# Performance work log

Measured on AMD Instinct MI355X. Metric: run time of the kernel, lower is better.

## Reference

```python
import jax, jax.numpy as jnp
import numpy as np

B, T, C = 2, 1024, 2048
HEAD = 64              # args.head_size_a
H = C // HEAD          # n_head = 32
D_DECAY, D_AAA, D_MV, D_GATE = 96, 96, 64, 256
GN_EPS = 0.00064
EPS_NORM = 1e-12

ARGS = ['x', 'v0', 'xx_r', 'xx_w', 'xx_k', 'xx_v', 'xx_a', 'xx_g',
        'ww_b', 'ww_w1', 'ww_w2', 'aa_b', 'aa_w1', 'aa_w2',
        'vv_b', 'vv_w1', 'vv_w2', 'gg_w1', 'gg_w2',
        'kk_s', 'ka_s', 'rk_s', 'W_r', 'W_k', 'W_v', 'W_o', 'gn_w', 'gn_b']


def setup_inputs() -> dict:
    key = jax.random.key(0)
    it = iter(jax.random.split(key, 32))
    nrm = lambda shape, s=1.0: jax.random.normal(next(it), shape, jnp.float32) * s
    d = {'x': nrm((B, T, C)), 'v0': nrm((B, T, C))}
    for nm in ('xx_r', 'xx_w', 'xx_k', 'xx_v', 'xx_a', 'xx_g',
               'ww_b', 'aa_b', 'vv_b', 'kk_s', 'ka_s'):
        d[nm] = nrm((1, 1, C), 0.5)
    d['ww_w1'] = nrm((C, D_DECAY), 0.02); d['ww_w2'] = nrm((D_DECAY, C), 0.02)
    d['aa_w1'] = nrm((C, D_AAA), 0.02);   d['aa_w2'] = nrm((D_AAA, C), 0.02)
    d['vv_w1'] = nrm((C, D_MV), 0.02);    d['vv_w2'] = nrm((D_MV, C), 0.02)
    d['gg_w1'] = nrm((C, D_GATE), 0.02);  d['gg_w2'] = nrm((D_GATE, C), 0.02)
    d['rk_s'] = nrm((H, HEAD), 0.5)
    d['W_r'] = nrm((C, C), 0.02); d['W_k'] = nrm((C, C), 0.02)
    d['W_v'] = nrm((C, C), 0.02); d['W_o'] = nrm((C, C), 0.02)
    d['gn_w'] = jnp.ones((C,), jnp.float32)
    d['gn_b'] = jnp.zeros((C,), jnp.float32)
    return d


def _rwkv7_op(r, w, k, v, a, b):
    # RWKV7 state recurrence: state[b,h,i,j] (i = value dim, j = key dim),
    # vectorized over (B,H,N), scanned over T.
    to_tbhn = lambda t: t.reshape(B, T, H, HEAD).astype(jnp.float32).transpose(1, 0, 2, 3)
    rT, kT, vT, aT, bT = map(to_tbhn, (r, k, v, a, b))
    wT = jnp.exp(-jnp.exp(to_tbhn(w)))   # decay in (0, 1)
    state0 = jnp.zeros((B, H, HEAD, HEAD), jnp.float32)

    def step(state, inp):
        wt, kt, vt, at, bt, rt = inp     # each [B,H,N]
        sa = jnp.einsum('bhij,bhj->bhi', state, at)
        state = (state * wt[:, :, None, :]
                 + sa[..., None] * bt[:, :, None, :]
                 + vt[..., None] * kt[:, :, None, :])
        return state, jnp.einsum('bhij,bhj->bhi', state, rt)

    _, outs = jax.lax.scan(step, state0, (wT, kT, vT, aT, bT, rT))  # [T,B,H,N]
    return outs.transpose(1, 0, 2, 3).reshape(B, T, C)


def _group_norm(y, gn_w, gn_b):
    # GroupNorm(H, C, eps=0.00064) applied on (B*T, C): per-(token, head) stats over N
    yh = y.reshape(B, T, H, HEAD)
    mu = yh.mean(-1, keepdims=True)
    var = yh.var(-1, keepdims=True)
    yh = (yh - mu) * jax.lax.rsqrt(var + GN_EPS)
    yh = yh * gn_w.reshape(1, 1, H, HEAD) + gn_b.reshape(1, 1, H, HEAD)
    return yh.reshape(B, T, C)


def _forward(x, v0, xx_r, xx_w, xx_k, xx_v, xx_a, xx_g,
             ww_b, ww_w1, ww_w2, aa_b, aa_w1, aa_w2,
             vv_b, vv_w1, vv_w2, gg_w1, gg_w2,
             kk_s, ka_s, rk_s, W_r, W_k, W_v, W_o, gn_w, gn_b):
    # time_shift(x) - x : shift sequence right by one with zero pad
    xx = jnp.pad(x, ((0, 0), (1, 0), (0, 0)))[:, :T, :] - x
    xr = x + xx * xx_r; xw = x + xx * xx_w; xk = x + xx * xx_k
    xv = x + xx * xx_v; xa = x + xx * xx_a; xg = x + xx * xx_g

    r = xr @ W_r
    w = -jax.nn.softplus(-(ww_b + jnp.tanh(xw @ ww_w1) @ ww_w2)) - 0.5  # clamp to (-inf,-0.5)
    k = xk @ W_k
    v = xv @ W_v
    # layer_id > 0: mix with layer-0 value residual
    v = v + (v0 - v) * jax.nn.sigmoid(vv_b + (xv @ vv_w1) @ vv_w2)
    a = jax.nn.sigmoid(aa_b + (xa @ aa_w1) @ aa_w2)
    g = jax.nn.sigmoid(xg @ gg_w1) @ gg_w2

    kk = k * kk_s
    kkh = kk.reshape(B, T, H, HEAD)
    kk = (kkh / jnp.maximum(jnp.linalg.norm(kkh, axis=-1, keepdims=True), EPS_NORM)).reshape(B, T, C)
    k = k * (1.0 + (a - 1.0) * ka_s)

    y = _rwkv7_op(r, w, k, v, -kk, kk * a)
    y = _group_norm(y, gn_w, gn_b)
    # per-head bonus: (r*k*rk_s).sum(-1) * v
    bonus = ((r.reshape(B, T, H, HEAD) * k.reshape(B, T, H, HEAD) * rk_s).sum(-1, keepdims=True)
             * v.reshape(B, T, H, HEAD)).reshape(B, T, C)
    y = y + bonus
    return (y * g) @ W_o


def reference(x, v0, xx_r, xx_w, xx_k, xx_v, xx_a, xx_g,
              ww_b, ww_w1, ww_w2, aa_b, aa_w1, aa_w2,
              vv_b, vv_w1, vv_w2, gg_w1, gg_w2,
              kk_s, ka_s, rk_s, W_r, W_k, W_v, W_o, gn_w, gn_b):
    out = _forward(x, v0, xx_r, xx_w, xx_k, xx_v, xx_a, xx_g,
                   ww_b, ww_w1, ww_w2, aa_b, aa_w1, aa_w2,
                   vv_b, vv_w1, vv_w2, gg_w1, gg_w2,
                   kk_s, ka_s, rk_s, W_r, W_k, W_v, W_o, gn_w, gn_b)
    # layer_id > 0 passes v0 through unchanged
    return (out, v0)
```

## Files before the change

### kernel.cpp

```cpp
#include <hip/hip_runtime.h>
#include <hip/hip_bf16.h>
#include <math.h>

typedef unsigned short u16;
typedef __attribute__((ext_vector_type(4))) unsigned short us4;
typedef __attribute__((ext_vector_type(8))) unsigned short us8;
typedef __attribute__((ext_vector_type(8))) short s8v;
typedef __attribute__((ext_vector_type(4))) float f4v;

#define BB 2
#define TT 1024
#define CC 2048
#define HH 32
#define BT (BB*TT)


__device__ __forceinline__ float bf2f(u16 u) {
  return __uint_as_float(((unsigned int)u) << 16);
}
__device__ __forceinline__ u16 f2bf(float f) {
  unsigned int x = __float_as_uint(f);
  x += 0x7fffu + ((x >> 16) & 1u);
  return (u16)(x >> 16);
}

__device__ __forceinline__ void gload16(const u16* g, u16* l) {
  __builtin_amdgcn_global_load_lds(
      (const __attribute__((address_space(1))) void*)g,
      (__attribute__((address_space(3))) void*)l, 16, 0, 0);
}

__global__ __launch_bounds__(256)
void mix_k(const float* __restrict__ x, const float* __restrict__ s,
           u16* __restrict__ out) {
  int idx = blockIdx.x * 256 + threadIdx.x;
  int c = idx & (CC - 1);
  int t = (idx >> 11) & (TT - 1);
  float xv = x[idx];
  float xp = (t == 0) ? 0.f : x[idx - CC];
  out[idx] = f2bf(xv + (xp - xv) * s[c]);
}

__global__ __launch_bounds__(256)
void wt_k(const float* __restrict__ W, u16* __restrict__ Wt, int K, int N,
          int Kp) {
  __shared__ u16 tile[32][36];
  const int k0 = blockIdx.x * 32, n0 = blockIdx.y * 32;
  const int tid = threadIdx.x;
  const int r = tid >> 3, c4 = (tid & 7) << 2;
  float4 v = *(const float4*)(W + (size_t)(k0 + r) * N + n0 + c4);
  tile[r][c4 + 0] = f2bf(v.x); tile[r][c4 + 1] = f2bf(v.y);
  tile[r][c4 + 2] = f2bf(v.z); tile[r][c4 + 3] = f2bf(v.w);
  __syncthreads();
  ushort4 o;
  o.x = tile[c4 + 0][r]; o.y = tile[c4 + 1][r];
  o.z = tile[c4 + 2][r]; o.w = tile[c4 + 3][r];
  *(ushort4*)(Wt + (size_t)(n0 + r) * Kp + k0 + c4) = o;
}

enum { EPI_BF = 0, EPI_F32 = 1, EPI_BIAS_SP = 2, EPI_BIAS_SIG = 3,
       EPI_VMIX = 4 };

template<int EPI>
__global__ __launch_bounds__(256)
void mgemm_k(const u16* __restrict__ A, const u16* __restrict__ Bt,
             float* __restrict__ outF, u16* __restrict__ outB,
             int M, int N, int K, int lda, int ldb,
             const float* __restrict__ bias, const u16* __restrict__ p1,
             const float* __restrict__ p2)
{
  __shared__ alignas(16) u16 As[128 * 64];
  __shared__ alignas(16) u16 Bs[128 * 64];
  const int m0 = blockIdx.x * 128;
  const int n0 = blockIdx.y * 128;
  const int tid = threadIdx.x;
  const int lane = tid & 63;
  const int wid = tid >> 6;
  const int wr = wid >> 1, wc = wid & 1;
  f4v acc[4][4];
  #pragma unroll
  for (int i = 0; i < 4; ++i)
    #pragma unroll
    for (int j = 0; j < 4; ++j) acc[i][j] = f4v{0.f, 0.f, 0.f, 0.f};

  const int l15 = lane & 15;
  const int lq = lane >> 4;
  const int nkt = K >> 6;
  for (int kt = 0; kt < nkt; ++kt) {
    const int k0 = kt << 6;
    __syncthreads();
    #pragma unroll
    for (int a = 0; a < 4; ++a) {
      const int blkU = (wid * 4 + a) * 64;
      const int U = blkU + lane;
      const int row = U >> 3;
      const int u = U & 7;
      const int col = ((u ^ (row & 7)) << 3);
      gload16(A  + (size_t)(m0 + row) * lda + k0 + col, &As[blkU * 8]);
      gload16(Bt + (size_t)(n0 + row) * ldb + k0 + col, &Bs[blkU * 8]);
    }
    __syncthreads();
    #pragma unroll
    for (int h = 0; h < 2; ++h) {
      s8v af[4], bfr[4];
      #pragma unroll
      for (int i = 0; i < 4; ++i) {
        const int row = wr * 64 + i * 16 + l15;
        const int u = (h * 4 + lq) ^ (row & 7);
        af[i] = *(const s8v*)&As[row * 64 + u * 8];
      }
      #pragma unroll
      for (int j = 0; j < 4; ++j) {
        const int row = wc * 64 + j * 16 + l15;
        const int u = (h * 4 + lq) ^ (row & 7);
        bfr[j] = *(const s8v*)&Bs[row * 64 + u * 8];
      }
      #pragma unroll
      for (int i = 0; i < 4; ++i)
        #pragma unroll
        for (int j = 0; j < 4; ++j)
          acc[i][j] = __builtin_amdgcn_mfma_f32_16x16x32_bf16(af[i], bfr[j],
                                                              acc[i][j],
                                                              0, 0, 0);
    }
  }
  const int rbase = m0 + wr * 64 + (lq << 2);
  const int cbase = n0 + wc * 64 + l15;
  #pragma unroll
  for (int i = 0; i < 4; ++i) {
    #pragma unroll
    for (int j = 0; j < 4; ++j) {
      f4v c = acc[i][j];
      const int col = cbase + j * 16;
      #pragma unroll
      for (int q = 0; q < 4; ++q) {
        const int row = rbase + i * 16 + q;
        const size_t idx = (size_t)row * N + col;
        const float r = c[q];
        if (EPI == EPI_BF) {
          outB[idx] = f2bf(r);
        } else if (EPI == EPI_F32) {
          outF[idx] = r;
        } else if (EPI == EPI_BIAS_SP) {
          float u = bias[col] + r;
          float z = -u;
          float sp = fmaxf(z, 0.f) + log1pf(expf(-fabsf(z)));
          outB[idx] = f2bf(-sp - 0.5f);
        } else if (EPI == EPI_BIAS_SIG) {
          float u = bias[col] + r;
          outB[idx] = f2bf(1.f / (1.f + expf(-u)));
        } else if (EPI == EPI_VMIX) {
          float u = bias[col] + r;
          float sg = 1.f / (1.f + expf(-u));
          float v = bf2f(p1[idx]);
          float v0v = p2[idx];
          outB[idx] = f2bf(v + (v0v - v) * sg);
        }
      }
    }
  }
}

__global__ __launch_bounds__(256)
void gemm_part_k(const u16* __restrict__ A, const float* __restrict__ W,
                 float* __restrict__ outF, int M, int N, int K, int kchunk,
                 int NP)
{
  __shared__ alignas(16) float As[16][68];
  __shared__ alignas(16) float Bs[16][68];
  const int m0 = blockIdx.x * 64;
  const int n0 = blockIdx.y * 64;
  const int kz = blockIdx.z;
  const int k0base = kz * kchunk;
  const int tid = threadIdx.x;
  const int tx = tid & 15, ty = tid >> 4;
  float acc[4][4] = {{0.f}};
  const int a_m = tid >> 2;
  const int a_k = (tid & 3) << 2;
  const int b_k = tid >> 4;
  const int b_n = (tid & 15) << 2;
  const int niters = kchunk >> 4;
  for (int it = 0; it < niters; ++it) {
    const int k0 = k0base + (it << 4);
    float4 av;
    {
      ushort4 u = *(const ushort4*)(A + (size_t)(m0 + a_m) * K + (k0 + a_k));
      av = make_float4(bf2f(u.x), bf2f(u.y), bf2f(u.z), bf2f(u.w));
    }
    float4 bv;
    {
      int gn = n0 + b_n;
      const float* wp = W + (size_t)(k0 + b_k) * N + gn;
      if (gn + 3 < N) {
        bv = *(const float4*)wp;
      } else {
        bv.x = (gn + 0 < N) ? wp[0] : 0.f;
        bv.y = (gn + 1 < N) ? wp[1] : 0.f;
        bv.z = (gn + 2 < N) ? wp[2] : 0.f;
        bv.w = (gn + 3 < N) ? wp[3] : 0.f;
      }
    }
    __syncthreads();
    As[a_k + 0][a_m] = av.x; As[a_k + 1][a_m] = av.y;
    As[a_k + 2][a_m] = av.z; As[a_k + 3][a_m] = av.w;
    Bs[b_k][b_n + 0] = bv.x; Bs[b_k][b_n + 1] = bv.y;
    Bs[b_k][b_n + 2] = bv.z; Bs[b_k][b_n + 3] = bv.w;
    __syncthreads();
    #pragma unroll
    for (int kk = 0; kk < 16; ++kk) {
      float4 a4 = *(const float4*)&As[kk][ty << 2];
      float4 b4 = *(const float4*)&Bs[kk][tx << 2];
      float ar[4] = {a4.x, a4.y, a4.z, a4.w};
      float br[4] = {b4.x, b4.y, b4.z, b4.w};
      #pragma unroll
      for (int i = 0; i < 4; ++i)
        #pragma unroll
        for (int j = 0; j < 4; ++j)
          acc[i][j] = fmaf(ar[i], br[j], acc[i][j]);
    }
  }
  #pragma unroll
  for (int i = 0; i < 4; ++i) {
    int gm = m0 + (ty << 2) + i;
    #pragma unroll
    for (int j = 0; j < 4; ++j) {
      int gn = n0 + (tx << 2) + j;
      if (gn >= N) continue;
      outF[((size_t)kz * M + gm) * NP + gn] = acc[i][j];
    }
  }
}

__global__ __launch_bounds__(256)
void reduce_k(const float* __restrict__ part, u16* __restrict__ out,
              int M, int D, int NP, int nz, int act, int Dp)
{
  int idx = blockIdx.x * 256 + threadIdx.x;
  if (idx >= M * Dp) return;
  int t = idx / Dp, n = idx - t * Dp;
  float s = 0.f;
  if (n < D) {
    for (int z = 0; z < nz; ++z) s += part[((size_t)z * M + t) * NP + n];
    if (act == 1) s = tanhf(s);
    else if (act == 2) s = 1.f / (1.f + expf(-s));
  }
  out[idx] = f2bf(s);
}

__global__ __launch_bounds__(256)
void prep_k(const u16* __restrict__ k_in, const u16* __restrict__ a_in,
            const u16* __restrict__ r_in, const u16* __restrict__ w_in,
            const float* __restrict__ kk_s, const float* __restrict__ ka_s,
            u16* __restrict__ ao_out, u16* __restrict__ bo_out,
            u16* __restrict__ k_out, u16* __restrict__ wd_out,
            u16* __restrict__ rw_out, float2* __restrict__ scal)
{
  int tid = threadIdx.x;
  int lane = tid & 63;
  int wv = tid >> 6;
  int hidx = blockIdx.x * 4 + wv;
  int h = hidx & (HH - 1);
  int c = (h << 6) + lane;
  size_t base = ((size_t)hidx << 6) + lane;
  float k = bf2f(k_in[base]);
  float kk = k * kk_s[c];
  float ss = kk * kk;
  for (int off = 32; off; off >>= 1) ss += __shfl_xor(ss, off, 64);
  float kkn = kk / fmaxf(sqrtf(ss), 1e-12f);
  float a = bf2f(a_in[base]);
  float r = bf2f(r_in[base]);
  float kf = k * (1.f + (a - 1.f) * ka_s[c]);
  float wd = expf(-expf(bf2f(w_in[base])));
  float bo = kkn * a;
  ao_out[base] = f2bf(-kkn);
  bo_out[base] = f2bf(bo);
  k_out[base]  = f2bf(kf);
  wd_out[base] = f2bf(wd);
  rw_out[base] = f2bf(wd * r);
  float kr = kf * r, br = bo * r;
  kr += __shfl_xor(kr, 1, 64);  br += __shfl_xor(br, 1, 64);
  kr += __shfl_xor(kr, 2, 64);  br += __shfl_xor(br, 2, 64);
  kr += __shfl_xor(kr, 4, 64);  br += __shfl_xor(br, 4, 64);
  kr += __shfl_xor(kr, 8, 64);  br += __shfl_xor(br, 8, 64);
  kr += __shfl_xor(kr, 16, 64); br += __shfl_xor(br, 16, 64);
  kr += __shfl_xor(kr, 32, 64); br += __shfl_xor(br, 32, 64);
  if (lane == 0) scal[hidx] = make_float2(kr, br);
}

__global__ __launch_bounds__(256)
void prep2_k(u16* __restrict__ wd, u16* __restrict__ ao,
             u16* __restrict__ bo, u16* __restrict__ rw,
             const u16* __restrict__ kf, float4* __restrict__ scal4)
{
  int tid = threadIdx.x;
  int lane = tid & 63;
  int wv = tid >> 6;
  int hpidx = blockIdx.x * 4 + wv;
  int h = hpidx & (HH - 1);
  int btp = hpidx >> 5;
  int tp = btp & (TT / 2 - 1);
  int b = btp >> 9;
  size_t be = ((size_t)(b * TT + 2 * tp)) * CC + (h << 6) + lane;
  size_t bodd = be + CC;
  float wd1 = bf2f(wd[be]),  wd2 = bf2f(wd[bodd]);
  float ao2 = bf2f(ao[bodd]), rw2 = bf2f(rw[bodd]);
  float bo1 = bf2f(bo[be]),  k1  = bf2f(kf[be]);
  float cba = bo1 * ao2, ckb = k1 * ao2, crb = bo1 * rw2, crk = k1 * rw2;
  #pragma unroll
  for (int off = 32; off; off >>= 1) {
    cba += __shfl_xor(cba, off, 64);
    ckb += __shfl_xor(ckb, off, 64);
    crb += __shfl_xor(crb, off, 64);
    crk += __shfl_xor(crk, off, 64);
  }
  wd[be]   = f2bf(wd1 * wd2);
  wd[bodd] = f2bf(k1 * wd2);
  ao[bodd] = f2bf(wd1 * ao2);
  bo[be]   = f2bf(bo1 * wd2);
  rw[bodd] = f2bf(wd1 * rw2);
  if (lane == 0) scal4[hpidx] = make_float4(cba, ckb, crb, crk);
}

__global__ __launch_bounds__(256)
void rec_k(const u16* __restrict__ rw, const u16* __restrict__ wd,
           const u16* __restrict__ kv, const u16* __restrict__ v,
           const u16* __restrict__ ao, const u16* __restrict__ bo,
           const float2* __restrict__ scal, const float4* __restrict__ scal4,
           u16* __restrict__ y)
{
  const int gw = blockIdx.x * 4 + (threadIdx.x >> 6);
  const int lane = threadIdx.x & 63;
  const int sub = lane & 15;
  const int grp = lane >> 4;
  const int bh = gw >> 4;
  const int rblk = gw & 15;
  const int i = rblk * 4 + grp;
  const int b = bh >> 5, h = bh & (HH - 1);
  const size_t base0 = ((size_t)b * TT) * CC + (h << 6);
  const size_t vecb = base0 + (sub << 2);
  const size_t vb   = base0 + i;
  const int sbase = b * TT * HH + h;
  const int pbase = b * (TT / 2) * HH + h;
  float s0 = 0.f, s1 = 0.f, s2 = 0.f, s3 = 0.f;

  us4 W12, KW1, AO1, WA2, BW1, BO2, RW1, WR2, K2;
  float V1, V2; float2 SE, SO; float4 S4;
#define PLOAD(TP) do {                                                  \
    const size_t be_ = vecb + (size_t)(2 * (TP)) * CC;                  \
    const size_t bo_ = be_ + CC;                                        \
    W12 = *(const us4*)(wd + be_);  KW1 = *(const us4*)(wd + bo_);      \
    AO1 = *(const us4*)(ao + be_);  WA2 = *(const us4*)(ao + bo_);      \
    BW1 = *(const us4*)(bo + be_);  BO2 = *(const us4*)(bo + bo_);      \
    RW1 = *(const us4*)(rw + be_);  WR2 = *(const us4*)(rw + bo_);      \
    K2  = *(const us4*)(kv + bo_);                                      \
    V1 = bf2f(v[vb + (size_t)(2 * (TP)) * CC]);                         \
    V2 = bf2f(v[vb + (size_t)(2 * (TP) + 1) * CC]);                     \
    SE = scal[sbase + (2 * (TP)) * HH];                                 \
    SO = scal[sbase + (2 * (TP) + 1) * HH];                             \
    S4 = scal4[pbase + (TP) * HH];                                      \
  } while (0)

  PLOAD(0);
  for (int tp = 0; tp < TT / 2; ++tp) {
    const float w0 = bf2f(W12[0]), w1 = bf2f(W12[1]),
                w2 = bf2f(W12[2]), w3 = bf2f(W12[3]);
    const float kw0 = bf2f(KW1[0]), kw1_ = bf2f(KW1[1]),
                kw2 = bf2f(KW1[2]), kw3 = bf2f(KW1[3]);
    const float a0 = bf2f(AO1[0]), a1 = bf2f(AO1[1]),
                a2 = bf2f(AO1[2]), a3 = bf2f(AO1[3]);
    const float x0 = bf2f(WA2[0]), x1 = bf2f(WA2[1]),
                x2 = bf2f(WA2[2]), x3 = bf2f(WA2[3]);
    const float bw0 = bf2f(BW1[0]), bw1_ = bf2f(BW1[1]),
                bw2 = bf2f(BW1[2]), bw3 = bf2f(BW1[3]);
    const float b0 = bf2f(BO2[0]), b1 = bf2f(BO2[1]),
                b2 = bf2f(BO2[2]), b3 = bf2f(BO2[3]);
    const float e0 = bf2f(RW1[0]), e1 = bf2f(RW1[1]),
                e2 = bf2f(RW1[2]), e3 = bf2f(RW1[3]);
    const float f0 = bf2f(WR2[0]), f1 = bf2f(WR2[1]),
                f2 = bf2f(WR2[2]), f3 = bf2f(WR2[3]);
    const float k0 = bf2f(K2[0]), k1 = bf2f(K2[1]),
                k2 = bf2f(K2[2]), k3 = bf2f(K2[3]);
    const float v1c = V1, v2c = V2;
    const float kr1 = SE.x, br1 = SE.y, kr2 = SO.x, br2 = SO.y;
    const float cba = S4.x, ckb = S4.y, crb = S4.z, crk = S4.w;
    if (tp + 1 < TT / 2) PLOAD(tp + 1);
    float u1 = fmaf(s3, a3, fmaf(s2, a2, fmaf(s1, a1, s0 * a0)));
    float u2 = fmaf(s3, x3, fmaf(s2, x2, fmaf(s1, x1, s0 * x0)));
    float q1 = fmaf(s3, e3, fmaf(s2, e2, fmaf(s1, e1, s0 * e0)));
    float q2 = fmaf(s3, f3, fmaf(s2, f2, fmaf(s1, f1, s0 * f0)));
    u1 += __shfl_xor(u1, 1, 64);  u2 += __shfl_xor(u2, 1, 64);
    q1 += __shfl_xor(q1, 1, 64);  q2 += __shfl_xor(q2, 1, 64);
    u1 += __shfl_xor(u1, 2, 64);  u2 += __shfl_xor(u2, 2, 64);
    q1 += __shfl_xor(q1, 2, 64);  q2 += __shfl_xor(q2, 2, 64);
    u1 += __shfl_xor(u1, 4, 64);  u2 += __shfl_xor(u2, 4, 64);
    q1 += __shfl_xor(q1, 4, 64);  q2 += __shfl_xor(q2, 4, 64);
    u1 += __shfl_xor(u1, 8, 64);  u2 += __shfl_xor(u2, 8, 64);
    q1 += __shfl_xor(q1, 8, 64);  q2 += __shfl_xor(q2, 8, 64);
    const float sac = fmaf(ckb, v1c, fmaf(cba, u1, u2));
    const float y1 = fmaf(br1, u1, fmaf(kr1, v1c, q1));
    const float y2 = fmaf(br2, sac, fmaf(kr2, v2c,
                       fmaf(crb, u1, fmaf(crk, v1c, q2))));
    s0 = fmaf(v2c, k0, fmaf(v1c, kw0, fmaf(sac, b0, fmaf(u1, bw0, s0 * w0))));
    s1 = fmaf(v2c, k1, fmaf(v1c, kw1_, fmaf(sac, b1, fmaf(u1, bw1_, s1 * w1))));
    s2 = fmaf(v2c, k2, fmaf(v1c, kw2, fmaf(sac, b2, fmaf(u1, bw2, s2 * w2))));
    s3 = fmaf(v2c, k3, fmaf(v1c, kw3, fmaf(sac, b3, fmaf(u1, bw3, s3 * w3))));
    if (sub == 0) {
      y[vb + (size_t)(2 * tp) * CC] = f2bf(y1);
      y[vb + (size_t)(2 * tp + 1) * CC] = f2bf(y2);
    }
  }
#undef PLOAD
}

__global__ __launch_bounds__(256)
void gn_k(u16* __restrict__ y, const u16* __restrict__ r,
          const u16* __restrict__ k, const u16* __restrict__ v,
          const u16* __restrict__ g, const float* __restrict__ rk_s,
          const float* __restrict__ gn_w, const float* __restrict__ gn_b)
{
  int tid = threadIdx.x, lane = tid & 63, wv = tid >> 6;
  int hidx = blockIdx.x * 4 + wv;
  int h = hidx & (HH - 1);
  int c = (h << 6) + lane;
  size_t base = ((size_t)hidx << 6) + lane;
  float yv = bf2f(y[base]), rv = bf2f(r[base]), kv = bf2f(k[base]);
  float vv = bf2f(v[base]), gv = bf2f(g[base]);
  float bsum = rv * kv * rk_s[c];
  float s1 = yv, s2 = yv * yv;
  for (int off = 32; off; off >>= 1) {
    s1 += __shfl_xor(s1, off, 64);
    s2 += __shfl_xor(s2, off, 64);
    bsum += __shfl_xor(bsum, off, 64);
  }
  float mu = s1 * (1.f / 64.f);
  float var = s2 * (1.f / 64.f) - mu * mu;
  float rstd = rsqrtf(var + 0.00064f);
  float z = (yv - mu) * rstd * gn_w[c] + gn_b[c];
  y[base] = f2bf((z + bsum * vv) * gv);
}

__global__ __launch_bounds__(256)
void copy_v0(const float* __restrict__ v0, float* __restrict__ out) {
  int idx = blockIdx.x * 256 + threadIdx.x;
  ((float4*)out)[idx] = ((const float4*)v0)[idx];
}

__global__ __launch_bounds__(256)
void zero_out(float* __restrict__ out) {
  int idx = blockIdx.x * 256 + threadIdx.x;
  ((float4*)out)[idx] = make_float4(0.f, 0.f, 0.f, 0.f);
}

extern "C" void kernel_launch(void* const* d_in, const int* in_sizes, int n_in,
                              void* d_out, int out_size, void* d_ws, size_t ws_size,
                              hipStream_t stream) {
  (void)n_in; (void)out_size;
  const bool dictOrder = (in_sizes[9] == CC);
  int IX[28];
  if (dictOrder) {
    const int m[28] = {0,1,2,3,4,5,6,7, 8,13,14, 9,15,16, 10,17,18, 19,20,
                       11,12,21, 22,23,24,25, 26,27};
    for (int i = 0; i < 28; ++i) IX[i] = m[i];
  } else {
    for (int i = 0; i < 28; ++i) IX[i] = i;
  }
  const float* x     = (const float*)d_in[IX[0]];
  const float* v0    = (const float*)d_in[IX[1]];
  const float* xx_r  = (const float*)d_in[IX[2]];
  const float* xx_w  = (const float*)d_in[IX[3]];
  const float* xx_k  = (const float*)d_in[IX[4]];
  const float* xx_v  = (const float*)d_in[IX[5]];
  const float* xx_a  = (const float*)d_in[IX[6]];
  const float* xx_g  = (const float*)d_in[IX[7]];
  const float* ww_b  = (const float*)d_in[IX[8]];
  const float* ww_w1 = (const float*)d_in[IX[9]];
  const float* ww_w2 = (const float*)d_in[IX[10]];
  const float* aa_b  = (const float*)d_in[IX[11]];
  const float* aa_w1 = (const float*)d_in[IX[12]];
  const float* aa_w2 = (const float*)d_in[IX[13]];
  const float* vv_b  = (const float*)d_in[IX[14]];
  const float* vv_w1 = (const float*)d_in[IX[15]];
  const float* vv_w2 = (const float*)d_in[IX[16]];
  const float* gg_w1 = (const float*)d_in[IX[17]];
  const float* gg_w2 = (const float*)d_in[IX[18]];
  const float* kk_s  = (const float*)d_in[IX[19]];
  const float* ka_s  = (const float*)d_in[IX[20]];
  const float* rk_s  = (const float*)d_in[IX[21]];
  const float* W_r   = (const float*)d_in[IX[22]];
  const float* W_k   = (const float*)d_in[IX[23]];
  const float* W_v   = (const float*)d_in[IX[24]];
  const float* W_o   = (const float*)d_in[IX[25]];
  const float* gn_w  = (const float*)d_in[IX[26]];
  const float* gn_b  = (const float*)d_in[IX[27]];

  const size_t NBTC = (size_t)BT * CC;
  dim3 blk(256);
  const int grid4f = (int)(NBTC / 4 / 256);

  const size_t WS_NEED = 7 * NBTC * sizeof(u16);
  float* outF = (float*)d_out;
  if (ws_size < WS_NEED || d_ws == nullptr) {
    zero_out<<<grid4f, blk, 0, stream>>>(outF);
    copy_v0<<<grid4f, blk, 0, stream>>>(v0, outF + NBTC);
    return;
  }

  u16* W16   = (u16*)d_ws;
  u16* R0 = W16 + 0 * NBTC;
  u16* R1 = W16 + 1 * NBTC;
  u16* R2 = W16 + 2 * NBTC;
  u16* R3 = W16 + 3 * NBTC;
  u16* R4 = W16 + 4 * NBTC;
  u16* R5 = W16 + 5 * NBTC;
  u16* R6 = W16 + 6 * NBTC;
  float* partY = (float*)R3;
  float* partG = (float*)R5;
  u16* ws_y = (u16*)(outF + NBTC);
  float2* scal = (float2*)(ws_y + NBTC);
  float4* scal4 = (float4*)(ws_y + NBTC + (size_t)BT * HH * 4);

  const int gridMix = (BT * CC) / 256;
  dim3 gM(BT / 128, 2048 / 128);

  mix_k<<<gridMix, blk, 0, stream>>>(x, xx_w, R6);
  gemm_part_k<<<dim3(32, 2, 8), blk, 0, stream>>>(R6, ww_w1, partY,
      BT, 96, 2048, 256, 128);
  reduce_k<<<(BT * 128) / 256, blk, 0, stream>>>(partY, R0, BT, 96, 128, 8, 1, 128);
  wt_k<<<dim3(3, 64), blk, 0, stream>>>(ww_w2, R1, 96, 2048, 128);
  mgemm_k<EPI_BIAS_SP><<<gM, blk, 0, stream>>>(R0, R1, nullptr, R5,
      BT, 2048, 128, 128, 128, ww_b, nullptr, nullptr);

  mix_k<<<gridMix, blk, 0, stream>>>(x, xx_a, R6);
  gemm_part_k<<<dim3(32, 2, 8), blk, 0, stream>>>(R6, aa_w1, partY,
      BT, 96, 2048, 256, 128);
  reduce_k<<<(BT * 128) / 256, blk, 0, stream>>>(partY, R0, BT, 96, 128, 8, 0, 128);
  wt_k<<<dim3(3, 64), blk, 0, stream>>>(aa_w2, R1, 96, 2048, 128);
  mgemm_k<EPI_BIAS_SIG><<<gM, blk, 0, stream>>>(R0, R1, nullptr, R4,
      BT, 2048, 128, 128, 128, aa_b, nullptr, nullptr);

  mix_k<<<gridMix, blk, 0, stream>>>(x, xx_v, R6);
  wt_k<<<dim3(64, 64), blk, 0, stream>>>(W_v, R1, 2048, 2048, 2048);
  mgemm_k<EPI_BF><<<gM, blk, 0, stream>>>(R6, R1, nullptr, R2,
      BT, 2048, 2048, 2048, 2048, nullptr, nullptr, nullptr);
  gemm_part_k<<<dim3(32, 1, 8), blk, 0, stream>>>(R6, vv_w1, partY,
      BT, 64, 2048, 256, 64);
  reduce_k<<<(BT * 64) / 256, blk, 0, stream>>>(partY, R0, BT, 64, 64, 8, 0, 64);
  wt_k<<<dim3(2, 64), blk, 0, stream>>>(vv_w2, R1, 64, 2048, 64);
  mgemm_k<EPI_VMIX><<<gM, blk, 0, stream>>>(R0, R1, nullptr, R2,
      BT, 2048, 64, 64, 64, vv_b, R2, v0);

  mix_k<<<gridMix, blk, 0, stream>>>(x, xx_k, R6);
  wt_k<<<dim3(64, 64), blk, 0, stream>>>(W_k, R3, 2048, 2048, 2048);
  mgemm_k<EPI_BF><<<gM, blk, 0, stream>>>(R6, R3, nullptr, R1,
      BT, 2048, 2048, 2048, 2048, nullptr, nullptr, nullptr);

  mix_k<<<gridMix, blk, 0, stream>>>(x, xx_r, R6);
  wt_k<<<dim3(64, 64), blk, 0, stream>>>(W_r, R3, 2048, 2048, 2048);
  mgemm_k<EPI_BF><<<gM, blk, 0, stream>>>(R6, R3, nullptr, R0,
      BT, 2048, 2048, 2048, 2048, nullptr, nullptr, nullptr);

  prep_k<<<BT * HH / 4, blk, 0, stream>>>(R1, R4, R0, R5, kk_s, ka_s,
                                          R3, R4, R1, R5, R6, scal);

  prep2_k<<<BT / 2 * HH / 4, blk, 0, stream>>>(R5, R3, R4, R6, R1, scal4);

  rec_k<<<256, blk, 0, stream>>>(R6, R5, R1, R2, R3, R4, scal, scal4, ws_y);

  mix_k<<<gridMix, blk, 0, stream>>>(x, xx_g, R6);
  gemm_part_k<<<dim3(32, 4, 2), blk, 0, stream>>>(R6, gg_w1, partG,
      BT, 256, 2048, 1024, 256);
  reduce_k<<<(BT * 256) / 256, blk, 0, stream>>>(partG, R3, BT, 256, 256, 2, 2, 256);
  wt_k<<<dim3(8, 64), blk, 0, stream>>>(gg_w2, R5, 256, 2048, 256);
  mgemm_k<EPI_BF><<<gM, blk, 0, stream>>>(R3, R5, nullptr, R4,
      BT, 2048, 256, 256, 256, nullptr, nullptr, nullptr);

  gn_k<<<BT * HH / 4, blk, 0, stream>>>(ws_y, R0, R1, R2, R4,
                                        rk_s, gn_w, gn_b);

  wt_k<<<dim3(64, 64), blk, 0, stream>>>(W_o, R5, 2048, 2048, 2048);
  mgemm_k<EPI_F32><<<gM, blk, 0, stream>>>(ws_y, R5, outF, nullptr,
      BT, 2048, 2048, 2048, 2048, nullptr, nullptr, nullptr);

  copy_v0<<<grid4f, blk, 0, stream>>>(v0, outF + NBTC);
}
```

Before: 809.3 us.

## Chunk the RWKV7 recurrence over four timesteps instead of two

The prep pass now precombines decay, key and a/b vectors over blocks of four timesteps and precomputes 24 cross-step scalar dot products per head. The recurrence kernel then advances the state four steps per iteration, halving the number of serial loop iterations and shuffle-reduction rounds on the critical path. The cost is more loads and registers per iteration, a heavier prep kernel, and extra bf16 rounding from products of several decays.

```diff
diff --git a/kernel.cpp b/kernel.cpp
--- a/kernel.cpp
+++ b/kernel.cpp
@@ -288,44 +288,88 @@
 }
 
 __global__ __launch_bounds__(256)
-void prep2_k(u16* __restrict__ wd, u16* __restrict__ ao,
-             u16* __restrict__ bo, u16* __restrict__ rw,
-             const u16* __restrict__ kf, float4* __restrict__ scal4)
+void prep4_k(u16* __restrict__ wd, u16* __restrict__ ao,
+             u16* __restrict__ bo, const u16* __restrict__ kv,
+             u16* __restrict__ rw, float4* __restrict__ sc24)
 {
-  int tid = threadIdx.x;
-  int lane = tid & 63;
-  int wv = tid >> 6;
-  int hpidx = blockIdx.x * 4 + wv;
-  int h = hpidx & (HH - 1);
-  int btp = hpidx >> 5;
-  int tp = btp & (TT / 2 - 1);
-  int b = btp >> 9;
-  size_t be = ((size_t)(b * TT + 2 * tp)) * CC + (h << 6) + lane;
-  size_t bodd = be + CC;
-  float wd1 = bf2f(wd[be]),  wd2 = bf2f(wd[bodd]);
-  float ao2 = bf2f(ao[bodd]), rw2 = bf2f(rw[bodd]);
-  float bo1 = bf2f(bo[be]),  k1  = bf2f(kf[be]);
-  float cba = bo1 * ao2, ckb = k1 * ao2, crb = bo1 * rw2, crk = k1 * rw2;
+  const int tid = threadIdx.x;
+  const int lane = tid & 63;
+  const int hq = blockIdx.x * 4 + (tid >> 6);
+  const int h = hq & (HH - 1);
+  const int bq = hq >> 5;
+  const int quad = bq & 255;
+  const int b = bq >> 8;
+  const size_t e0 = ((size_t)(b * TT + 4 * quad)) * CC + (h << 6) + lane;
+  const size_t e1 = e0 + CC, e2 = e0 + 2 * CC, e3 = e0 + 3 * CC;
+  const float w1 = bf2f(wd[e0]), w2 = bf2f(wd[e1]),
+              w3 = bf2f(wd[e2]), w4 = bf2f(wd[e3]);
+  const float a2 = bf2f(ao[e1]), a3 = bf2f(ao[e2]), a4 = bf2f(ao[e3]);
+  const float b1 = bf2f(bo[e0]), b2 = bf2f(bo[e1]), b3 = bf2f(bo[e2]);
+  const float k1 = bf2f(kv[e0]), k2 = bf2f(kv[e1]), k3 = bf2f(kv[e2]);
+  const float r2 = bf2f(rw[e1]), r3 = bf2f(rw[e2]), r4 = bf2f(rw[e3]);
+  const float cw1 = w1, cw2 = cw1 * w2, cw3 = cw2 * w3, Wc = cw3 * w4;
+  const float sw4 = w4, sw3 = w3 * w4, sw2 = w2 * sw3;
+  const float w23 = w2 * w3;
+  float sred[24];
+  sred[0]  = b1 * a2;
+  sred[1]  = b1 * w2 * a3;
+  sred[2]  = b2 * a3;
+  sred[3]  = b1 * w23 * a4;
+  sred[4]  = b2 * w3 * a4;
+  sred[5]  = b3 * a4;
+  sred[6]  = k1 * a2;
+  sred[7]  = k1 * w2 * a3;
+  sred[8]  = k2 * a3;
+  sred[9]  = k1 * w23 * a4;
+  sred[10] = k2 * w3 * a4;
+  sred[11] = k3 * a4;
+  sred[12] = b1 * r2;
+  sred[13] = b1 * w2 * r3;
+  sred[14] = b2 * r3;
+  sred[15] = b1 * w23 * r4;
+  sred[16] = b2 * w3 * r4;
+  sred[17] = b3 * r4;
+  sred[18] = k1 * r2;
+  sred[19] = k1 * w2 * r3;
+  sred[20] = k2 * r3;
+  sred[21] = k1 * w23 * r4;
+  sred[22] = k2 * w3 * r4;
+  sred[23] = k3 * r4;
   #pragma unroll
-  for (int off = 32; off; off >>= 1) {
-    cba += __shfl_xor(cba, off, 64);
-    ckb += __shfl_xor(ckb, off, 64);
-    crb += __shfl_xor(crb, off, 64);
-    crk += __shfl_xor(crk, off, 64);
-  }
-  wd[be]   = f2bf(wd1 * wd2);
-  wd[bodd] = f2bf(k1 * wd2);
-  ao[bodd] = f2bf(wd1 * ao2);
-  bo[be]   = f2bf(bo1 * wd2);
-  rw[bodd] = f2bf(wd1 * rw2);
-  if (lane == 0) scal4[hpidx] = make_float4(cba, ckb, crb, crk);
+  for (int lv = 0; lv < 6; ++lv) {
+    const int off = 1 << lv;
+    #pragma unroll
+    for (int i = 0; i < 24; ++i) sred[i] += __shfl_xor(sred[i], off, 64);
+  }
+  wd[e0] = f2bf(Wc);
+  wd[e1] = f2bf(b1 * sw2);
+  wd[e2] = f2bf(b2 * sw3);
+  wd[e3] = f2bf(b3 * sw4);
+  ao[e1] = f2bf(cw1 * a2);
+  ao[e2] = f2bf(cw2 * a3);
+  ao[e3] = f2bf(cw3 * a4);
+  bo[e0] = f2bf(k1 * sw2);
+  bo[e1] = f2bf(k2 * sw3);
+  bo[e2] = f2bf(k3 * sw4);
+  rw[e1] = f2bf(cw1 * r2);
+  rw[e2] = f2bf(cw2 * r3);
+  rw[e3] = f2bf(cw3 * r4);
+  if (lane == 0) {
+    float4* p = sc24 + (size_t)hq * 6;
+    p[0] = make_float4(sred[0],  sred[1],  sred[2],  sred[3]);
+    p[1] = make_float4(sred[4],  sred[5],  sred[6],  sred[7]);
+    p[2] = make_float4(sred[8],  sred[9],  sred[10], sred[11]);
+    p[3] = make_float4(sred[12], sred[13], sred[14], sred[15]);
+    p[4] = make_float4(sred[16], sred[17], sred[18], sred[19]);
+    p[5] = make_float4(sred[20], sred[21], sred[22], sred[23]);
+  }
 }
 
 __global__ __launch_bounds__(256)
 void rec_k(const u16* __restrict__ rw, const u16* __restrict__ wd,
            const u16* __restrict__ kv, const u16* __restrict__ v,
            const u16* __restrict__ ao, const u16* __restrict__ bo,
-           const float2* __restrict__ scal, const float4* __restrict__ scal4,
+           const float2* __restrict__ scal, const float4* __restrict__ sc24,
            u16* __restrict__ y)
 {
   const int gw = blockIdx.x * 4 + (threadIdx.x >> 6);
@@ -340,73 +384,124 @@
   const size_t vecb = base0 + (sub << 2);
   const size_t vb   = base0 + i;
   const int sbase = b * TT * HH + h;
-  const int pbase = b * (TT / 2) * HH + h;
+  const int qbase = b * (TT / 4) * HH + h;
   float s0 = 0.f, s1 = 0.f, s2 = 0.f, s3 = 0.f;
 
-  us4 W12, KW1, AO1, WA2, BW1, BO2, RW1, WR2, K2;
-  float V1, V2; float2 SE, SO; float4 S4;
+  us4 Wv, B1v, B2v, B3v, B4v, M1v, M2v, M3v, M4v,
+      K1v, K2v, K3v, K4v, R1v, R2v, R3v, R4v;
+  float V1, V2, V3, V4;
+  float2 SE1, SE2, SE3, SE4;
+  float4 C0, C1, C2, C3, C4, C5;
 #define PLOAD(TP) do {                                                  \
-    const size_t be_ = vecb + (size_t)(2 * (TP)) * CC;                  \
-    const size_t bo_ = be_ + CC;                                        \
-    W12 = *(const us4*)(wd + be_);  KW1 = *(const us4*)(wd + bo_);      \
-    AO1 = *(const us4*)(ao + be_);  WA2 = *(const us4*)(ao + bo_);      \
-    BW1 = *(const us4*)(bo + be_);  BO2 = *(const us4*)(bo + bo_);      \
-    RW1 = *(const us4*)(rw + be_);  WR2 = *(const us4*)(rw + bo_);      \
-    K2  = *(const us4*)(kv + bo_);                                      \
-    V1 = bf2f(v[vb + (size_t)(2 * (TP)) * CC]);                         \
-    V2 = bf2f(v[vb + (size_t)(2 * (TP) + 1) * CC]);                     \
-    SE = scal[sbase + (2 * (TP)) * HH];                                 \
-    SO = scal[sbase + (2 * (TP) + 1) * HH];                             \
-    S4 = scal4[pbase + (TP) * HH];                                      \
+    const size_t e_ = vecb + (size_t)(4 * (TP)) * CC;                   \
+    Wv  = *(const us4*)(wd + e_);                                       \
+    B1v = *(const us4*)(wd + e_ + CC);                                  \
+    B2v = *(const us4*)(wd + e_ + 2 * CC);                              \
+    B3v = *(const us4*)(wd + e_ + 3 * CC);                              \
+    M1v = *(const us4*)(ao + e_);                                       \
+    M2v = *(const us4*)(ao + e_ + CC);                                  \
+    M3v = *(const us4*)(ao + e_ + 2 * CC);                              \
+    M4v = *(const us4*)(ao + e_ + 3 * CC);                              \
+    K1v = *(const us4*)(bo + e_);                                       \
+    K2v = *(const us4*)(bo + e_ + CC);                                  \
+    K3v = *(const us4*)(bo + e_ + 2 * CC);                              \
+    B4v = *(const us4*)(bo + e_ + 3 * CC);                              \
+    R1v = *(const us4*)(rw + e_);                                       \
+    R2v = *(const us4*)(rw + e_ + CC);                                  \
+    R3v = *(const us4*)(rw + e_ + 2 * CC);                              \
+    R4v = *(const us4*)(rw + e_ + 3 * CC);                              \
+    K4v = *(const us4*)(kv + e_ + 3 * CC);                              \
+    V1 = bf2f(v[vb + (size_t)(4 * (TP) + 0) * CC]);                     \
+    V2 = bf2f(v[vb + (size_t)(4 * (TP) + 1) * CC]);                     \
+    V3 = bf2f(v[vb + (size_t)(4 * (TP) + 2) * CC]);                     \
+    V4 = bf2f(v[vb + (size_t)(4 * (TP) + 3) * CC]);                     \
+    SE1 = scal[sbase + (4 * (TP) + 0) * HH];                            \
+    SE2 = scal[sbase + (4 * (TP) + 1) * HH];                            \
+    SE3 = scal[sbase + (4 * (TP) + 2) * HH];                            \
+    SE4 = scal[sbase + (4 * (TP) + 3) * HH];                            \
+    const float4* pp_ = sc24 + (size_t)(qbase + (TP) * HH) * 6;         \
+    C0 = pp_[0]; C1 = pp_[1]; C2 = pp_[2];                              \
+    C3 = pp_[3]; C4 = pp_[4]; C5 = pp_[5];                              \
   } while (0)
 
   PLOAD(0);
-  for (int tp = 0; tp < TT / 2; ++tp) {
-    const float w0 = bf2f(W12[0]), w1 = bf2f(W12[1]),
-                w2 = bf2f(W12[2]), w3 = bf2f(W12[3]);
-    const float kw0 = bf2f(KW1[0]), kw1_ = bf2f(KW1[1]),
-                kw2 = bf2f(KW1[2]), kw3 = bf2f(KW1[3]);
-    const float a0 = bf2f(AO1[0]), a1 = bf2f(AO1[1]),
-                a2 = bf2f(AO1[2]), a3 = bf2f(AO1[3]);
-    const float x0 = bf2f(WA2[0]), x1 = bf2f(WA2[1]),
-                x2 = bf2f(WA2[2]), x3 = bf2f(WA2[3]);
-    const float bw0 = bf2f(BW1[0]), bw1_ = bf2f(BW1[1]),
-                bw2 = bf2f(BW1[2]), bw3 = bf2f(BW1[3]);
-    const float b0 = bf2f(BO2[0]), b1 = bf2f(BO2[1]),
-                b2 = bf2f(BO2[2]), b3 = bf2f(BO2[3]);
-    const float e0 = bf2f(RW1[0]), e1 = bf2f(RW1[1]),
-                e2 = bf2f(RW1[2]), e3 = bf2f(RW1[3]);
-    const float f0 = bf2f(WR2[0]), f1 = bf2f(WR2[1]),
-                f2 = bf2f(WR2[2]), f3 = bf2f(WR2[3]);
-    const float k0 = bf2f(K2[0]), k1 = bf2f(K2[1]),
-                k2 = bf2f(K2[2]), k3 = bf2f(K2[3]);
-    const float v1c = V1, v2c = V2;
-    const float kr1 = SE.x, br1 = SE.y, kr2 = SO.x, br2 = SO.y;
-    const float cba = S4.x, ckb = S4.y, crb = S4.z, crk = S4.w;
-    if (tp + 1 < TT / 2) PLOAD(tp + 1);
-    float u1 = fmaf(s3, a3, fmaf(s2, a2, fmaf(s1, a1, s0 * a0)));
-    float u2 = fmaf(s3, x3, fmaf(s2, x2, fmaf(s1, x1, s0 * x0)));
-    float q1 = fmaf(s3, e3, fmaf(s2, e2, fmaf(s1, e1, s0 * e0)));
-    float q2 = fmaf(s3, f3, fmaf(s2, f2, fmaf(s1, f1, s0 * f0)));
-    u1 += __shfl_xor(u1, 1, 64);  u2 += __shfl_xor(u2, 1, 64);
-    q1 += __shfl_xor(q1, 1, 64);  q2 += __shfl_xor(q2, 1, 64);
-    u1 += __shfl_xor(u1, 2, 64);  u2 += __shfl_xor(u2, 2, 64);
-    q1 += __shfl_xor(q1, 2, 64);  q2 += __shfl_xor(q2, 2, 64);
-    u1 += __shfl_xor(u1, 4, 64);  u2 += __shfl_xor(u2, 4, 64);
-    q1 += __shfl_xor(q1, 4, 64);  q2 += __shfl_xor(q2, 4, 64);
-    u1 += __shfl_xor(u1, 8, 64);  u2 += __shfl_xor(u2, 8, 64);
-    q1 += __shfl_xor(q1, 8, 64);  q2 += __shfl_xor(q2, 8, 64);
-    const float sac = fmaf(ckb, v1c, fmaf(cba, u1, u2));
-    const float y1 = fmaf(br1, u1, fmaf(kr1, v1c, q1));
-    const float y2 = fmaf(br2, sac, fmaf(kr2, v2c,
-                       fmaf(crb, u1, fmaf(crk, v1c, q2))));
-    s0 = fmaf(v2c, k0, fmaf(v1c, kw0, fmaf(sac, b0, fmaf(u1, bw0, s0 * w0))));
-    s1 = fmaf(v2c, k1, fmaf(v1c, kw1_, fmaf(sac, b1, fmaf(u1, bw1_, s1 * w1))));
-    s2 = fmaf(v2c, k2, fmaf(v1c, kw2, fmaf(sac, b2, fmaf(u1, bw2, s2 * w2))));
-    s3 = fmaf(v2c, k3, fmaf(v1c, kw3, fmaf(sac, b3, fmaf(u1, bw3, s3 * w3))));
+  for (int tp = 0; tp < TT / 4; ++tp) {
+    float Wf[4], B1f[4], B2f[4], B3f[4], B4f[4],
+          M1f[4], M2f[4], M3f[4], M4f[4],
+          K1f[4], K2f[4], K3f[4], K4f[4],
+          R1f[4], R2f[4], R3f[4], R4f[4];
+    #pragma unroll
+    for (int e = 0; e < 4; ++e) {
+      Wf[e]  = bf2f(Wv[e]);  B1f[e] = bf2f(B1v[e]);
+      B2f[e] = bf2f(B2v[e]); B3f[e] = bf2f(B3v[e]);
+      B4f[e] = bf2f(B4v[e]);
+      M1f[e] = bf2f(M1v[e]); M2f[e] = bf2f(M2v[e]);
+      M3f[e] = bf2f(M3v[e]); M4f[e] = bf2f(M4v[e]);
+      K1f[e] = bf2f(K1v[e]); K2f[e] = bf2f(K2v[e]);
+      K3f[e] = bf2f(K3v[e]); K4f[e] = bf2f(K4v[e]);
+      R1f[e] = bf2f(R1v[e]); R2f[e] = bf2f(R2v[e]);
+      R3f[e] = bf2f(R3v[e]); R4f[e] = bf2f(R4v[e]);
+    }
+    const float v1c = V1, v2c = V2, v3c = V3, v4c = V4;
+    const float kr1 = SE1.x, br1 = SE1.y, kr2 = SE2.x, br2 = SE2.y;
+    const float kr3 = SE3.x, br3 = SE3.y, kr4 = SE4.x, br4 = SE4.y;
+    const float c21 = C0.x, c31 = C0.y, c32 = C0.z, c41 = C0.w;
+    const float c42 = C1.x, c43 = C1.y, d21 = C1.z, d31 = C1.w;
+    const float d32 = C2.x, d41 = C2.y, d42 = C2.z, d43 = C2.w;
+    const float p21 = C3.x, p31 = C3.y, p32 = C3.z, p41 = C3.w;
+    const float p42 = C4.x, p43 = C4.y, g21 = C4.z, g31 = C4.w;
+    const float g32 = C5.x, g41 = C5.y, g42 = C5.z, g43 = C5.w;
+    if (tp + 1 < TT / 4) PLOAD(tp + 1);
+    float u1 = fmaf(s3, M1f[3], fmaf(s2, M1f[2], fmaf(s1, M1f[1], s0 * M1f[0])));
+    float u2 = fmaf(s3, M2f[3], fmaf(s2, M2f[2], fmaf(s1, M2f[1], s0 * M2f[0])));
+    float u3 = fmaf(s3, M3f[3], fmaf(s2, M3f[2], fmaf(s1, M3f[1], s0 * M3f[0])));
+    float u4 = fmaf(s3, M4f[3], fmaf(s2, M4f[2], fmaf(s1, M4f[1], s0 * M4f[0])));
+    float q1 = fmaf(s3, R1f[3], fmaf(s2, R1f[2], fmaf(s1, R1f[1], s0 * R1f[0])));
+    float q2 = fmaf(s3, R2f[3], fmaf(s2, R2f[2], fmaf(s1, R2f[1], s0 * R2f[0])));
+    float q3 = fmaf(s3, R3f[3], fmaf(s2, R3f[2], fmaf(s1, R3f[1], s0 * R3f[0])));
+    float q4 = fmaf(s3, R4f[3], fmaf(s2, R4f[2], fmaf(s1, R4f[1], s0 * R4f[0])));
+    #pragma unroll
+    for (int lv = 0; lv < 4; ++lv) {
+      const int off = 1 << lv;
+      u1 += __shfl_xor(u1, off, 64);  u2 += __shfl_xor(u2, off, 64);
+      u3 += __shfl_xor(u3, off, 64);  u4 += __shfl_xor(u4, off, 64);
+      q1 += __shfl_xor(q1, off, 64);  q2 += __shfl_xor(q2, off, 64);
+      q3 += __shfl_xor(q3, off, 64);  q4 += __shfl_xor(q4, off, 64);
+    }
+    const float sa1 = u1;
+    const float sa2 = fmaf(d21, v1c, fmaf(c21, sa1, u2));
+    const float sa3 = fmaf(d32, v2c, fmaf(d31, v1c,
+                       fmaf(c32, sa2, fmaf(c31, sa1, u3))));
+    const float sa4 = fmaf(d43, v3c, fmaf(d42, v2c, fmaf(d41, v1c,
+                       fmaf(c43, sa3, fmaf(c42, sa2, fmaf(c41, sa1, u4))))));
+    const float y1 = fmaf(br1, sa1, fmaf(kr1, v1c, q1));
+    const float y2 = fmaf(br2, sa2, fmaf(kr2, v2c,
+                       fmaf(p21, sa1, fmaf(g21, v1c, q2))));
+    const float y3 = fmaf(br3, sa3, fmaf(kr3, v3c,
+                       fmaf(p31, sa1, fmaf(p32, sa2,
+                       fmaf(g31, v1c, fmaf(g32, v2c, q3))))));
+    const float y4 = fmaf(br4, sa4, fmaf(kr4, v4c,
+                       fmaf(p41, sa1, fmaf(p42, sa2, fmaf(p43, sa3,
+                       fmaf(g41, v1c, fmaf(g42, v2c, fmaf(g43, v3c, q4))))))));
+    float* sp[4] = {&s0, &s1, &s2, &s3};
+    #pragma unroll
+    for (int e = 0; e < 4; ++e) {
+      float sv = *sp[e] * Wf[e];
+      sv = fmaf(sa1, B1f[e], sv);
+      sv = fmaf(sa2, B2f[e], sv);
+      sv = fmaf(sa3, B3f[e], sv);
+      sv = fmaf(sa4, B4f[e], sv);
+      sv = fmaf(v1c, K1f[e], sv);
+      sv = fmaf(v2c, K2f[e], sv);
+      sv = fmaf(v3c, K3f[e], sv);
+      sv = fmaf(v4c, K4f[e], sv);
+      *sp[e] = sv;
+    }
     if (sub == 0) {
-      y[vb + (size_t)(2 * tp) * CC] = f2bf(y1);
-      y[vb + (size_t)(2 * tp + 1) * CC] = f2bf(y2);
+      y[vb + (size_t)(4 * tp + 0) * CC] = f2bf(y1);
+      y[vb + (size_t)(4 * tp + 1) * CC] = f2bf(y2);
+      y[vb + (size_t)(4 * tp + 2) * CC] = f2bf(y3);
+      y[vb + (size_t)(4 * tp + 3) * CC] = f2bf(y4);
     }
   }
 #undef PLOAD
@@ -517,7 +612,7 @@
   float* partG = (float*)R5;
   u16* ws_y = (u16*)(outF + NBTC);
   float2* scal = (float2*)(ws_y + NBTC);
-  float4* scal4 = (float4*)(ws_y + NBTC + (size_t)BT * HH * 4);
+  float4* sc24 = (float4*)(ws_y + NBTC + (size_t)BT * HH * 4);
 
   const int gridMix = (BT * CC) / 256;
   dim3 gM(BT / 128, 2048 / 128);
@@ -562,9 +657,10 @@
   prep_k<<<BT * HH / 4, blk, 0, stream>>>(R1, R4, R0, R5, kk_s, ka_s,
                                           R3, R4, R1, R5, R6, scal);
 
-  prep2_k<<<BT / 2 * HH / 4, blk, 0, stream>>>(R5, R3, R4, R6, R1, scal4);
-
-  rec_k<<<256, blk, 0, stream>>>(R6, R5, R1, R2, R3, R4, scal, scal4, ws_y);
+  prep4_k<<<(BB * (TT / 4) * HH) / 4, blk, 0, stream>>>(R5, R3, R4, R1, R6,
+                                                        sc24);
+
+  rec_k<<<256, blk, 0, stream>>>(R6, R5, R1, R2, R3, R4, scal, sc24, ws_y);
 
   mix_k<<<gridMix, blk, 0, stream>>>(x, xx_g, R6);
   gemm_part_k<<<dim3(32, 4, 2), blk, 0, stream>>>(R6, gg_w1, partG,
```

Result: slower. 846.3 us (+4.6%).
